# Kernel optimization log

Measured on AMD Instinct MI355X. Metric: run time of the kernel, lower is better.

Reference implementation:

```python
import jax, jax.numpy as jnp
import numpy as np

D, N = 512, 65536


def setup_inputs() -> dict:
    key = jax.random.key(0)
    k1, k2 = jax.random.split(key)
    feats = jax.random.normal(k1, (D, N), dtype=jnp.float32)
    warped_feats = jax.random.normal(k2, (D, N), dtype=jnp.float32)
    return {"feats": feats, "warped_feats": warped_feats}


def reference(feats, warped_feats):
    # diag(feats.T @ warped_feats)[n] == sum_d feats[d,n] * warped_feats[d,n]
    # Same math as the torch module, without materializing the NxN matrix.
    diag = jnp.einsum('dn,dn->n', feats, warped_feats)  # [N]
    cosine = 1.0 - diag
    return cosine.mean()
```

## Files before the change

### kernel.cpp

```cpp
#include <hip/hip_runtime.h>

#define THREADS 256
#define BLOCKS  2048
#define CHUNKS  16
#define PIPE    6

typedef float f32x4 __attribute__((ext_vector_type(4)));

__global__ __launch_bounds__(THREADS, 8) void dot_partial_kernel(
        const f32x4* __restrict__ a,
        const f32x4* __restrict__ b,
        float* __restrict__ partial) {
    const int base = blockIdx.x * (CHUNKS * THREADS) + threadIdx.x;

    f32x4 va[PIPE], vb[PIPE];

    #pragma unroll
    for (int i = 0; i < PIPE; ++i) {
        va[i] = __builtin_nontemporal_load(a + base + i * THREADS);
        vb[i] = __builtin_nontemporal_load(b + base + i * THREADS);
    }

    f32x4 acc0 = (f32x4)0.f, acc1 = (f32x4)0.f;

    #pragma unroll
    for (int i = 0; i < CHUNKS; ++i) {
        const int slot = i % PIPE;
        if (i & 1) acc1 += va[slot] * vb[slot];
        else       acc0 += va[slot] * vb[slot];
        if (i + PIPE < CHUNKS) {
            va[slot] = __builtin_nontemporal_load(a + base + (i + PIPE) * THREADS);
            vb[slot] = __builtin_nontemporal_load(b + base + (i + PIPE) * THREADS);
        }
    }

    f32x4 accv = acc0 + acc1;
    float s = (accv.x + accv.y) + (accv.z + accv.w);

    #pragma unroll
    for (int off = 32; off > 0; off >>= 1)
        s += __shfl_down(s, off, 64);

    __shared__ float smem[THREADS / 64];
    const int lane = threadIdx.x & 63;
    const int wave = threadIdx.x >> 6;
    if (lane == 0) smem[wave] = s;
    __syncthreads();

    if (threadIdx.x == 0) {
        float t = 0.f;
        #pragma unroll
        for (int w = 0; w < THREADS / 64; ++w) t += smem[w];
        partial[blockIdx.x] = t;
    }
}

__global__ __launch_bounds__(256) void final_reduce_kernel(
        const float* __restrict__ partial,
        float* __restrict__ out,
        int np, float inv_n) {
    float s = 0.f;
    for (int i = threadIdx.x; i < np; i += 256) s += partial[i];

    #pragma unroll
    for (int off = 32; off > 0; off >>= 1)
        s += __shfl_down(s, off, 64);

    __shared__ float smem[4];
    const int lane = threadIdx.x & 63;
    const int wave = threadIdx.x >> 6;
    if (lane == 0) smem[wave] = s;
    __syncthreads();

    if (threadIdx.x == 0) {
        float t = 0.f;
        #pragma unroll
        for (int w = 0; w < 4; ++w) t += smem[w];
        out[0] = 1.0f - t * inv_n;
    }
}

extern "C" void kernel_launch(void* const* d_in, const int* in_sizes, int n_in,
                              void* d_out, int out_size, void* d_ws, size_t ws_size,
                              hipStream_t stream) {
    const float* feats  = (const float*)d_in[0];
    const float* warped = (const float*)d_in[1];
    float* out = (float*)d_out;
    float* ws  = (float*)d_ws;

    const float inv_n = 1.0f / 65536.0f;

    dot_partial_kernel<<<BLOCKS, THREADS, 0, stream>>>(
        (const f32x4*)feats, (const f32x4*)warped, ws);
    final_reduce_kernel<<<1, 256, 0, stream>>>(ws, out, BLOCKS, inv_n);
}
```

Before: 249.0 us.

## Stream last four chunks per wave via direct global-to-LDS loads

Each wave now owns a contiguous run of 16 chunks. The first 12 are loaded into registers with the existing nontemporal pipeline, and the last 4 are fetched directly into LDS with global_load_lds at kernel start. This raises the number of bytes in flight per wave without adding register pressure, to better saturate HBM bandwidth. It adds 32KB of LDS per block, which may cap occupancy, and it drops the occupancy hint from launch_bounds. The global access order also changes from block-strided to wave-contiguous.

```diff
diff --git a/kernel.cpp b/kernel.cpp
--- a/kernel.cpp
+++ b/kernel.cpp
@@ -1,37 +1,63 @@
 #include <hip/hip_runtime.h>
 
-#define THREADS 256
-#define BLOCKS  2048
-#define CHUNKS  16
-#define PIPE    6
+#define THREADS   256
+#define BLOCKS    2048
+#define CHUNKS    16
+#define NT_CHUNKS 12
+#define PIPE      6
 
 typedef float f32x4 __attribute__((ext_vector_type(4)));
 
-__global__ __launch_bounds__(THREADS, 8) void dot_partial_kernel(
+__global__ __launch_bounds__(THREADS) void dot_partial_kernel(
         const f32x4* __restrict__ a,
         const f32x4* __restrict__ b,
         float* __restrict__ partial) {
-    const int base = blockIdx.x * (CHUNKS * THREADS) + threadIdx.x;
+    __shared__ __align__(16) char lds[4][4][2048];
+    __shared__ float smem_red[4];
+
+    const int wave = threadIdx.x >> 6;
+    const int lane = threadIdx.x & 63;
+    const long long wc0 = ((long long)blockIdx.x * 4 + wave) * CHUNKS;
 
     f32x4 va[PIPE], vb[PIPE];
+    #pragma unroll
+    for (int i = 0; i < PIPE; ++i) {
+        const long long g = (wc0 + i) * 64 + lane;
+        va[i] = __builtin_nontemporal_load(a + g);
+        vb[i] = __builtin_nontemporal_load(b + g);
+    }
 
     #pragma unroll
-    for (int i = 0; i < PIPE; ++i) {
-        va[i] = __builtin_nontemporal_load(a + base + i * THREADS);
-        vb[i] = __builtin_nontemporal_load(b + base + i * THREADS);
+    for (int c = 0; c < 4; ++c) {
+        const long long g = (wc0 + NT_CHUNKS + c) * 64 + lane;
+        __builtin_amdgcn_global_load_lds(
+            (const __attribute__((address_space(1))) void*)(a + g),
+            (__attribute__((address_space(3))) void*)&lds[wave][c][0], 16, 0, 0);
+        __builtin_amdgcn_global_load_lds(
+            (const __attribute__((address_space(1))) void*)(b + g),
+            (__attribute__((address_space(3))) void*)&lds[wave][c][1024], 16, 0, 0);
     }
 
     f32x4 acc0 = (f32x4)0.f, acc1 = (f32x4)0.f;
-
     #pragma unroll
-    for (int i = 0; i < CHUNKS; ++i) {
+    for (int i = 0; i < NT_CHUNKS; ++i) {
         const int slot = i % PIPE;
         if (i & 1) acc1 += va[slot] * vb[slot];
         else       acc0 += va[slot] * vb[slot];
-        if (i + PIPE < CHUNKS) {
-            va[slot] = __builtin_nontemporal_load(a + base + (i + PIPE) * THREADS);
-            vb[slot] = __builtin_nontemporal_load(b + base + (i + PIPE) * THREADS);
+        if (i + PIPE < NT_CHUNKS) {
+            const long long g = (wc0 + i + PIPE) * 64 + lane;
+            va[slot] = __builtin_nontemporal_load(a + g);
+            vb[slot] = __builtin_nontemporal_load(b + g);
         }
+    }
+
+    __asm__ volatile("s_waitcnt vmcnt(0)" ::: "memory");
+    #pragma unroll
+    for (int c = 0; c < 4; ++c) {
+        f32x4 av = *(const f32x4*)&lds[wave][c][lane * 16];
+        f32x4 bv = *(const f32x4*)&lds[wave][c][1024 + lane * 16];
+        if (c & 1) acc1 += av * bv;
+        else       acc0 += av * bv;
     }
 
     f32x4 accv = acc0 + acc1;
@@ -41,16 +67,13 @@
     for (int off = 32; off > 0; off >>= 1)
         s += __shfl_down(s, off, 64);
 
-    __shared__ float smem[THREADS / 64];
-    const int lane = threadIdx.x & 63;
-    const int wave = threadIdx.x >> 6;
-    if (lane == 0) smem[wave] = s;
+    if (lane == 0) smem_red[wave] = s;
     __syncthreads();
 
     if (threadIdx.x == 0) {
         float t = 0.f;
         #pragma unroll
-        for (int w = 0; w < THREADS / 64; ++w) t += smem[w];
+        for (int w = 0; w < 4; ++w) t += smem_red[w];
         partial[blockIdx.x] = t;
     }
 }
```

New measurement: 256.1 us. 2.8% more time.
